# Optimization experiments

Measured on AMD Instinct MI355X. Metric: run time of the kernel, lower is better.

Reference implementation:

```python
import jax, jax.numpy as jnp
import numpy as np

D = 1024
N_HEADS = 16
HEAD = D // N_HEADS


def apply_rope(x):
    # x: [b, h, s, hd]
    b, h, s, hd = x.shape
    half = hd // 2
    pos = jnp.arange(1, s + 1, dtype=jnp.float32)  # positions start at 1 (as in source)
    thetas = 10000.0 ** (-2.0 * jnp.arange(half, dtype=jnp.float32) / hd)
    angles = pos[:, None] * thetas[None, :]  # [s, half]
    cos, sin = jnp.cos(angles), jnp.sin(angles)
    x_even, x_odd = x[..., 0::2], x[..., 1::2]
    out_even = x_even * cos - x_odd * sin
    out_odd = x_odd * cos + x_even * sin
    # interleave back: stack on new last axis then reshape
    return jnp.stack([out_even, out_odd], axis=-1).reshape(b, h, s, hd)


def setup_inputs() -> dict:
    key = jax.random.key(0)
    k1, k2, k3 = jax.random.split(key, 3)
    b, s = 4, 2048
    x = jax.random.normal(k1, (b, s, D), dtype=jnp.float32)
    # torch Linear(d, 3d, bias=False): y = x @ W.T; store as [d, 3d] so y = x @ W_qkv
    W_qkv = jax.random.normal(k2, (D, 3 * D), dtype=jnp.float32) * (1.0 / np.sqrt(D))
    W_out = jax.random.normal(k3, (D, D), dtype=jnp.float32) * (1.0 / np.sqrt(D))
    return {"x": x, "W_qkv": W_qkv, "W_out": W_out}


def reference(x, W_qkv, W_out):
    b, s, _ = x.shape
    qkv = x @ W_qkv  # [b, s, 3d]
    q, k, v = jnp.split(qkv, 3, axis=-1)

    def split_heads(t):
        return t.reshape(b, s, N_HEADS, HEAD).transpose(0, 2, 1, 3)  # [b,h,s,hd]

    q, k, v = split_heads(q), split_heads(k), split_heads(v)
    q, k = apply_rope(q), apply_rope(k)
    scale = 1.0 / np.sqrt(HEAD)
    scores = jnp.einsum("bhqd,bhkd->bhqk", q, k) * scale
    attn = jax.nn.softmax(scores, axis=-1)
    out = jnp.einsum("bhqk,bhkd->bhqd", attn, v)  # [b,h,s,hd]
    out = out.transpose(0, 2, 1, 3).reshape(b, s, D)
    return out @ W_out
```

## Files before the change

kernel.cpp:

```cpp
#include <hip/hip_runtime.h>
#include <hip/hip_bf16.h>
#include <math.h>

#define BB 4
#define SS 2048
#define DD 1024
#define NH 16
#define HD 64

typedef __attribute__((ext_vector_type(8))) short bf16x8;
typedef __attribute__((ext_vector_type(4))) float f32x4;

#define MFMA16(a, b, c) __builtin_amdgcn_mfma_f32_16x16x32_bf16(a, b, c, 0, 0, 0)

#if __has_builtin(__builtin_amdgcn_exp2f)
#define EXP2(x) __builtin_amdgcn_exp2f(x)
#else
#define EXP2(x) exp2f(x)
#endif

__device__ __forceinline__ ushort f2bf(float f) {
    unsigned int u = __builtin_bit_cast(unsigned int, f);
    u += 0x7FFF + ((u >> 16) & 1);
    return (ushort)(u >> 16);
}
__device__ __forceinline__ float bf2f(ushort u) {
    return __builtin_bit_cast(float, (unsigned)u << 16);
}
__device__ __forceinline__ unsigned pk2bf(float a, float b) {
    __hip_bfloat162 h = __float22bfloat162_rn(make_float2(a, b));
    unsigned r;
    __builtin_memcpy(&r, &h, 4);
    return r;
}

__device__ __forceinline__ void gload16(const void* g, void* l) {
    __builtin_amdgcn_global_load_lds(
        (const __attribute__((address_space(1))) void*)g,
        (__attribute__((address_space(3))) void*)l, 16, 0, 0);
}

__global__ __launch_bounds__(256)
void prep_kernel(const float* __restrict__ X, ushort* __restrict__ Xb,
                 const float* __restrict__ Wqkv, ushort* __restrict__ Wqt,
                 const float* __restrict__ Wout, ushort* __restrict__ Wot,
                 float2* __restrict__ tab)
{
    const int blk = blockIdx.x;
    const int t = threadIdx.x;
    if (blk < 4096) {
        const size_t i = ((size_t)blk * 256 + t) * 8;
        const float4 v0 = *(const float4*)&X[i];
        const float4 v1 = *(const float4*)&X[i + 4];
        uint4 o;
        o.x = pk2bf(v0.x, v0.y);
        o.y = pk2bf(v0.z, v0.w);
        o.z = pk2bf(v1.x, v1.y);
        o.w = pk2bf(v1.z, v1.w);
        *(uint4*)&Xb[i] = o;
    } else if (blk < 5120) {
        __shared__ ushort T[64][72];
        const bool isQ = blk < 4864;
        const int b2 = isQ ? blk - 4096 : blk - 4864;
        const int ncols = isQ ? 3072 : 1024;
        const float* W = isQ ? Wqkv : Wout;
        ushort* Wt = isQ ? Wqt : Wot;
        const int ki = b2 / (ncols / 64), ni = b2 % (ncols / 64);
        const int k0 = ki * 64, n0 = ni * 64;
        #pragma unroll
        for (int e = 0; e < 4; ++e) {
            const int idx = t + e * 256;
            const int kr = idx >> 4, c4 = (idx & 15) * 4;
            const float4 v = *(const float4*)&W[(size_t)(k0 + kr) * ncols + n0 + c4];
            T[c4 + 0][kr] = f2bf(v.x); T[c4 + 1][kr] = f2bf(v.y);
            T[c4 + 2][kr] = f2bf(v.z); T[c4 + 3][kr] = f2bf(v.w);
        }
        __syncthreads();
        #pragma unroll
        for (int e = 0; e < 2; ++e) {
            const int idx = t + e * 256;
            const int nr = idx >> 3, kc = (idx & 7) * 8;
            uint4 o;
            o.x = (unsigned)T[nr][kc + 0] | ((unsigned)T[nr][kc + 1] << 16);
            o.y = (unsigned)T[nr][kc + 2] | ((unsigned)T[nr][kc + 3] << 16);
            o.z = (unsigned)T[nr][kc + 4] | ((unsigned)T[nr][kc + 5] << 16);
            o.w = (unsigned)T[nr][kc + 6] | ((unsigned)T[nr][kc + 7] << 16);
            *(uint4*)&Wt[(size_t)(n0 + nr) * 1024 + k0 + kc] = o;
        }
    } else {
        const int id = (blk - 5120) * 256 + t;
        const int s = id >> 5, i = id & 31;
        const float theta = expf(-0.28782313662425572f * (float)i);
        const float ang = (float)(s + 1) * theta;
        float sn, cs;
        sincosf(ang, &sn, &cs);
        tab[id] = make_float2(cs, sn);
    }
}

__global__ __launch_bounds__(256)
void rope_cast_kernel(ushort* __restrict__ Qi, ushort* __restrict__ Ki,
                      const float2* __restrict__ tab)
{
    const int HALFT = BB * NH * SS * 8;
    const int tid = blockIdx.x * 256 + threadIdx.x;
    const bool isK = tid >= HALFT;
    const int rr = isK ? tid - HALFT : tid;
    ushort* buf = isK ? Ki : Qi;
    const float sc = isK ? 1.0f : 0.180336880111112f;

    const int row = rr >> 3;
    const int e8  = rr & 7;
    const int s   = row & (SS - 1);
    const size_t base = (size_t)row * HD + e8 * 8;
    const uint4 iv = *(const uint4*)&buf[base];
    const unsigned ua[4] = {iv.x, iv.y, iv.z, iv.w};

    uint4 o;
    unsigned ow[4];
    #pragma unroll
    for (int j = 0; j < 4; ++j) {
        const float xe = __builtin_bit_cast(float, ua[j] << 16);
        const float xo = __builtin_bit_cast(float, ua[j] & 0xffff0000u);
        const float2 cs = tab[s * 32 + e8 * 4 + j];
        const float oe = (xe * cs.x - xo * cs.y) * sc;
        const float oo = (xo * cs.x + xe * cs.y) * sc;
        ow[j] = pk2bf(oe, oo);
    }
    o.x = ow[0]; o.y = ow[1]; o.z = ow[2]; o.w = ow[3];
    *(uint4*)&buf[base] = o;
}

template<int K, int NI>
__global__ __launch_bounds__(256)
void gemm_bt_kernel(const ushort* __restrict__ Ag, const ushort* __restrict__ Btg,
                    ushort* __restrict__ D0, ushort* __restrict__ D1,
                    ushort* __restrict__ D2)
{
    __shared__ ushort Ab[2][128 * 32];
    __shared__ ushort Bb[2][128 * 32];
    const int t = threadIdx.x, lane = t & 63, w = t >> 6;
    const int lo = lane & 15, g = lane >> 4;
    const int wr = w >> 1, wc = w & 1;

    const int nwg = gridDim.x;
    const int bid = blockIdx.x;
    const int wg = (bid & 7) * (nwg >> 3) + (bid >> 3);
    const int m0 = (wg / NI) * 128, n0 = (wg % NI) * 128;

    const int srow  = lane >> 2;
    const int sslot = (lane & 3) ^ ((srow >> 1) & 3);

    f32x4 acc[4][4];
    #pragma unroll
    for (int m = 0; m < 4; ++m)
        #pragma unroll
        for (int n = 0; n < 4; ++n)
            acc[m][n] = (f32x4){0.f, 0.f, 0.f, 0.f};

#define STAGE(kt, bb)                                                              \
    {                                                                              \
        const int kk = (kt) * 32;                                                  \
        _Pragma("unroll")                                                          \
        for (int e = 0; e < 2; ++e) {                                              \
            const int r0 = w * 32 + e * 16;                                        \
            gload16(Ag  + (size_t)(m0 + r0 + srow) * K + kk + sslot * 8,           \
                    &Ab[bb][r0 * 32]);                                             \
            gload16(Btg + (size_t)(n0 + r0 + srow) * K + kk + sslot * 8,           \
                    &Bb[bb][r0 * 32]);                                             \
        }                                                                          \
    }

    const int NKS = K / 32;
    STAGE(0, 0)
    for (int kt = 0; kt < NKS; ++kt) {
        const int cur = kt & 1;
        if (kt + 1 < NKS) {
            STAGE(kt + 1, cur ^ 1)
            asm volatile("s_waitcnt vmcnt(4)" ::: "memory");
        } else {
            asm volatile("s_waitcnt vmcnt(0)" ::: "memory");
        }
        __builtin_amdgcn_sched_barrier(0);
        __builtin_amdgcn_s_barrier();

        const int xsl = ((g ^ ((lo >> 1) & 3)) << 3);
        bf16x8 af[4], bfr[4];
        #pragma unroll
        for (int m = 0; m < 4; ++m)
            af[m] = *(const bf16x8*)&Ab[cur][(wr * 64 + m * 16 + lo) * 32 + xsl];
        #pragma unroll
        for (int n = 0; n < 4; ++n)
            bfr[n] = *(const bf16x8*)&Bb[cur][(wc * 64 + n * 16 + lo) * 32 + xsl];
        #pragma unroll
        for (int m = 0; m < 4; ++m)
            #pragma unroll
            for (int n = 0; n < 4; ++n)
                acc[m][n] = MFMA16(af[m], bfr[n], acc[m][n]);

        asm volatile("s_waitcnt lgkmcnt(0)" ::: "memory");
        __builtin_amdgcn_sched_barrier(0);
        __builtin_amdgcn_s_barrier();
    }
#undef STAGE

    const int tensor = n0 >> 10;
    const int cb = n0 & 1023;
    if (tensor == 2) {
        #pragma unroll
        for (int m = 0; m < 4; ++m) {
            const int row0 = m0 + wr * 64 + m * 16 + g * 4;
            const int b = row0 >> 11, sbase = row0 & (SS - 1);
            #pragma unroll
            for (int n = 0; n < 4; ++n) {
                const int c = cb + wc * 64 + n * 16 + lo;
                const int h = c >> 6, d = c & 63;
                uint2 wv = make_uint2(pk2bf(acc[m][n][0], acc[m][n][1]),
                                      pk2bf(acc[m][n][2], acc[m][n][3]));
                *(uint2*)&D2[(((size_t)b * NH + h) * HD + d) * SS + sbase] = wv;
            }
        }
    } else {
        ushort* dst = (tensor == 0) ? D0 : D1;
        const bool evlane = (lo & 1) == 0;
        #pragma unroll
        for (int m = 0; m < 4; ++m)
            #pragma unroll
            for (int n = 0; n < 4; ++n) {
                const int c = cb + wc * 64 + n * 16 + lo;
                const int h = c >> 6, d = c & 63;
                #pragma unroll
                for (int r = 0; r < 4; ++r) {
                    const int row = m0 + wr * 64 + m * 16 + g * 4 + r;
                    const float x  = acc[m][n][r];
                    const float xp = __shfl_xor(x, 1);
                    if (evlane) {
                        const int b = row >> 11, s = row & (SS - 1);
                        *(unsigned*)&dst[(((size_t)b * NH + h) * SS + s) * HD + d] =
                            pk2bf(x, xp);
                    }
                }
            }
    }
}

template<int K>
__global__ __launch_bounds__(256)
void gemm_bt64_kernel(const ushort* __restrict__ Ag, const ushort* __restrict__ Btg,
                      float* __restrict__ Df)
{
    __shared__ ushort Ab[2][128 * 32];
    __shared__ ushort Bb[2][64 * 32];
    const int t = threadIdx.x, lane = t & 63, w = t >> 6;
    const int lo = lane & 15, g = lane >> 4;
    const int NI = 16;

    const int nwg = gridDim.x;
    const int bid = blockIdx.x;
    const int wg = (bid & 7) * (nwg >> 3) + (bid >> 3);
    const int m0 = (wg / NI) * 128, n0 = (wg % NI) * 64;

    const int srow  = lane >> 2;
    const int sslot = (lane & 3) ^ ((srow >> 1) & 3);

    f32x4 acc[2][4];
    #pragma unroll
    for (int m = 0; m < 2; ++m)
        #pragma unroll
        for (int n = 0; n < 4; ++n)
            acc[m][n] = (f32x4){0.f, 0.f, 0.f, 0.f};

#define STAGE(kt, bb)                                                              \
    {                                                                              \
        const int kk = (kt) * 32;                                                  \
        _Pragma("unroll")                                                          \
        for (int e = 0; e < 2; ++e) {                                              \
            const int r0 = w * 32 + e * 16;                                        \
            gload16(Ag + (size_t)(m0 + r0 + srow) * K + kk + sslot * 8,            \
                    &Ab[bb][r0 * 32]);                                             \
        }                                                                          \
        gload16(Btg + (size_t)(n0 + w * 16 + srow) * K + kk + sslot * 8,           \
                &Bb[bb][(w * 16) * 32]);                                           \
    }

    const int NKS = K / 32;
    STAGE(0, 0)
    for (int kt = 0; kt < NKS; ++kt) {
        const int cur = kt & 1;
        if (kt + 1 < NKS) {
            STAGE(kt + 1, cur ^ 1)
            asm volatile("s_waitcnt vmcnt(3)" ::: "memory");
        } else {
            asm volatile("s_waitcnt vmcnt(0)" ::: "memory");
        }
        __builtin_amdgcn_sched_barrier(0);
        __builtin_amdgcn_s_barrier();

        const int xsl = ((g ^ ((lo >> 1) & 3)) << 3);
        bf16x8 af[2], bfr[4];
        #pragma unroll
        for (int m = 0; m < 2; ++m)
            af[m] = *(const bf16x8*)&Ab[cur][(w * 32 + m * 16 + lo) * 32 + xsl];
        #pragma unroll
        for (int n = 0; n < 4; ++n)
            bfr[n] = *(const bf16x8*)&Bb[cur][(n * 16 + lo) * 32 + xsl];
        #pragma unroll
        for (int m = 0; m < 2; ++m)
            #pragma unroll
            for (int n = 0; n < 4; ++n)
                acc[m][n] = MFMA16(af[m], bfr[n], acc[m][n]);

        asm volatile("s_waitcnt lgkmcnt(0)" ::: "memory");
        __builtin_amdgcn_sched_barrier(0);
        __builtin_amdgcn_s_barrier();
    }
#undef STAGE

    const bool evlane = (lo & 1) == 0;
    #pragma unroll
    for (int m = 0; m < 2; ++m)
        #pragma unroll
        for (int n = 0; n < 4; ++n) {
            const int col = n0 + n * 16 + lo;
            #pragma unroll
            for (int r = 0; r < 4; ++r) {
                const int row = m0 + w * 32 + m * 16 + g * 4 + r;
                const float x  = acc[m][n][r];
                const float xp = __shfl_xor(x, 1);
                if (evlane)
                    *(float2*)&Df[(size_t)row * 1024 + col] = make_float2(x, xp);
            }
        }
}

__global__ __launch_bounds__(256, 4)
void attn_mfma_kernel(const ushort* __restrict__ Qbf, const ushort* __restrict__ Kbf,
                      const ushort* __restrict__ Vt, ushort* __restrict__ Obt)
{
    __shared__ ushort Ks[2][4096];
    __shared__ ushort Vs[2][4096];

    const int t    = threadIdx.x;
    const int lane = t & 63;
    const int w    = t >> 6;
    const int g    = lane >> 4;
    const int lo   = lane & 15;
    const int lo7  = lo & 7;

    const int i  = blockIdx.x;
    const int r_ = i & 63;
    const int bh = (r_ & 7) * 8 + (r_ >> 3);
    const int qt = i >> 6;

    const size_t kbase  = (size_t)bh * SS * HD;
    const size_t vtbase = (size_t)bh * HD * SS;
    const int s0 = qt * 128;

    bf16x8 qa[2][2];
    #pragma unroll
    for (int qh = 0; qh < 2; ++qh)
        #pragma unroll
        for (int df = 0; df < 2; ++df)
            qa[qh][df] = *(const bf16x8*)
                &Qbf[kbase + (size_t)(s0 + w * 32 + qh * 16 + lo) * HD + df * 32 + g * 8];

    f32x4 Oc[2][4];
    #pragma unroll
    for (int qh = 0; qh < 2; ++qh)
        #pragma unroll
        for (int nb = 0; nb < 4; ++nb)
            Oc[qh][nb] = (f32x4){0.f, 0.f, 0.f, 0.f};
    f32x4 lacc[2];
    lacc[0] = (f32x4){0.f, 0.f, 0.f, 0.f};
    lacc[1] = (f32x4){0.f, 0.f, 0.f, 0.f};
    const bf16x8 ones = {16256, 16256, 16256, 16256, 16256, 16256, 16256, 16256};

    const int srcsw = ((lane & 7) ^ (lane >> 3)) * 8;
    const int rowin = (lane >> 3);

    #define STAGE(kt, bb)                                                          \
    {                                                                              \
        _Pragma("unroll")                                                          \
        for (int e = 0; e < 2; ++e) {                                              \
            const int rw = w * 16 + e * 8;                                         \
            gload16(&Kbf[kbase + (size_t)((kt) * 64 + rw + rowin) * HD + srcsw],   \
                    &Ks[bb][rw * 64]);                                             \
            gload16(&Vt[vtbase + (size_t)(rw + rowin) * SS + (kt) * 64 + srcsw],   \
                    &Vs[bb][rw * 64]);                                             \
        }                                                                          \
    }

    const int NT = SS / 64;
    STAGE(0, 0)

    for (int kt = 0; kt < NT; ++kt) {
        const int cur = kt & 1;
        if (kt + 1 < NT) {
            STAGE(kt + 1, cur ^ 1)
            asm volatile("s_waitcnt vmcnt(4)" ::: "memory");
        } else {
            asm volatile("s_waitcnt vmcnt(0)" ::: "memory");
        }
        __builtin_amdgcn_sched_barrier(0);
        __builtin_amdgcn_s_barrier();

        f32x4 St[2][4];
        __builtin_amdgcn_s_setprio(1);
        #pragma unroll
        for (int k16 = 0; k16 < 4; ++k16) {
            const int row = k16 * 16 + lo;
            const int cb = row * 64;
            const bf16x8 k0 = *(const bf16x8*)&Ks[cur][cb + (((0 + g) ^ lo7) * 8)];
            const bf16x8 k1 = *(const bf16x8*)&Ks[cur][cb + (((4 + g) ^ lo7) * 8)];
            const f32x4 z = {0.f, 0.f, 0.f, 0.f};
            St[0][k16] = MFMA16(k0, qa[0][0], z);
            St[0][k16] = MFMA16(k1, qa[0][1], St[0][k16]);
            St[1][k16] = MFMA16(k0, qa[1][0], z);
            St[1][k16] = MFMA16(k1, qa[1][1], St[1][k16]);
        }
        __builtin_amdgcn_s_setprio(0);

        #pragma unroll
        for (int qh = 0; qh < 2; ++qh)
            #pragma unroll
            for (int k16 = 0; k16 < 4; ++k16)
                #pragma unroll
                for (int r = 0; r < 4; ++r)
                    St[qh][k16][r] = EXP2(St[qh][k16][r]);

        #pragma unroll
        for (int ph = 0; ph < 2; ++ph) {
            bf16x8 vf[4];
            #pragma unroll
            for (int nb = 0; nb < 4; ++nb) {
                const int rb = (nb * 16 + lo) * 64 + (g & 1) * 4;
                const uint2 vlo = *(const uint2*)
                    &Vs[cur][rb + (((ph * 4 + (g >> 1)) ^ lo7) * 8)];
                const uint2 vhi = *(const uint2*)
                    &Vs[cur][rb + (((ph * 4 + (g >> 1) + 2) ^ lo7) * 8)];
                const uint4 vv = make_uint4(vlo.x, vlo.y, vhi.x, vhi.y);
                __builtin_memcpy(&vf[nb], &vv, 16);
            }
            __builtin_amdgcn_s_setprio(1);
            #pragma unroll
            for (int qh = 0; qh < 2; ++qh) {
                uint4 pu;
                pu.x = pk2bf(St[qh][2 * ph][0], St[qh][2 * ph][1]);
                pu.y = pk2bf(St[qh][2 * ph][2], St[qh][2 * ph][3]);
                pu.z = pk2bf(St[qh][2 * ph + 1][0], St[qh][2 * ph + 1][1]);
                pu.w = pk2bf(St[qh][2 * ph + 1][2], St[qh][2 * ph + 1][3]);
                bf16x8 pa;
                __builtin_memcpy(&pa, &pu, 16);
                lacc[qh] = MFMA16(pa, ones, lacc[qh]);
                #pragma unroll
                for (int nb = 0; nb < 4; ++nb)
                    Oc[qh][nb] = MFMA16(pa, vf[nb], Oc[qh][nb]);
            }
            __builtin_amdgcn_s_setprio(0);
        }

        asm volatile("s_waitcnt lgkmcnt(0)" ::: "memory");
        __builtin_amdgcn_sched_barrier(0);
        __builtin_amdgcn_s_barrier();
    }

    const int b = bh >> 4, h = bh & 15;
    #pragma unroll
    for (int qh = 0; qh < 2; ++qh) {
        #pragma unroll
        for (int r = 0; r < 4; ++r) {
            const float inv = 1.0f / lacc[qh][r];
            const int srow = s0 + w * 32 + qh * 16 + g * 4 + r;
            const size_t rbase = (size_t)(b * SS + srow) * 1024 + h * HD;
            #pragma unroll
            for (int nb = 0; nb < 4; ++nb)
                Obt[rbase + nb * 16 + lo] = f2bf(Oc[qh][nb][r] * inv);
        }
    }
    #undef STAGE
}

extern "C" void kernel_launch(void* const* d_in, const int* in_sizes, int n_in,
                              void* d_out, int out_size, void* d_ws, size_t ws_size,
                              hipStream_t stream)
{
    const float* x    = (const float*)d_in[0];
    const float* Wqkv = (const float*)d_in[1];
    const float* Wout = (const float*)d_in[2];
    float* out = (float*)d_out;

    const size_t TEN = (size_t)BB * NH * SS * HD;
    ushort* u = (ushort*)d_ws;
    ushort* Qb16 = u;
    ushort* Kb16 = u + TEN;
    ushort* Vt   = u + 2 * TEN;
    ushort* Obt  = u + 3 * TEN;
    ushort* Xb   = u + 4 * TEN;
    ushort* Wqt  = u + 5 * TEN;
    ushort* Wot  = u + 5 * TEN + 3145728;
    float2* tab  = (float2*)(u + 5 * TEN + 3145728 + 1048576);

    prep_kernel<<<dim3(4096 + 768 + 256 + 256), 256, 0, stream>>>(
        x, Xb, Wqkv, Wqt, Wout, Wot, tab);

    gemm_bt_kernel<1024, 24><<<dim3(64 * 24), 256, 0, stream>>>(
        Xb, Wqt, Qb16, Kb16, Vt);

    rope_cast_kernel<<<dim3(2 * BB * NH * SS * 8 / 256), 256, 0, stream>>>(
        Qb16, Kb16, tab);

    attn_mfma_kernel<<<dim3(BB * NH * (SS / 128)), 256, 0, stream>>>(
        Qb16, Kb16, Vt, Obt);

    gemm_bt64_kernel<1024><<<dim3(64 * 16), 256, 0, stream>>>(Obt, Wot, out);
}
```

Before: 209.0 us.

## Fuse Q RoPE into attention kernel and pad LDS rows for K/V tiles

```diff
diff --git a/kernel.cpp b/kernel.cpp
--- a/kernel.cpp
+++ b/kernel.cpp
@@ -99,21 +99,14 @@
 }
 
 __global__ __launch_bounds__(256)
-void rope_cast_kernel(ushort* __restrict__ Qi, ushort* __restrict__ Ki,
-                      const float2* __restrict__ tab)
+void rope_k_kernel(ushort* __restrict__ Ki, const float2* __restrict__ tab)
 {
-    const int HALFT = BB * NH * SS * 8;
-    const int tid = blockIdx.x * 256 + threadIdx.x;
-    const bool isK = tid >= HALFT;
-    const int rr = isK ? tid - HALFT : tid;
-    ushort* buf = isK ? Ki : Qi;
-    const float sc = isK ? 1.0f : 0.180336880111112f;
-
+    const int rr = blockIdx.x * 256 + threadIdx.x;
     const int row = rr >> 3;
     const int e8  = rr & 7;
     const int s   = row & (SS - 1);
     const size_t base = (size_t)row * HD + e8 * 8;
-    const uint4 iv = *(const uint4*)&buf[base];
+    const uint4 iv = *(const uint4*)&Ki[base];
     const unsigned ua[4] = {iv.x, iv.y, iv.z, iv.w};
 
     uint4 o;
@@ -123,12 +116,12 @@
         const float xe = __builtin_bit_cast(float, ua[j] << 16);
         const float xo = __builtin_bit_cast(float, ua[j] & 0xffff0000u);
         const float2 cs = tab[s * 32 + e8 * 4 + j];
-        const float oe = (xe * cs.x - xo * cs.y) * sc;
-        const float oo = (xo * cs.x + xe * cs.y) * sc;
+        const float oe = xe * cs.x - xo * cs.y;
+        const float oo = xo * cs.x + xe * cs.y;
         ow[j] = pk2bf(oe, oo);
     }
     o.x = ow[0]; o.y = ow[1]; o.z = ow[2]; o.w = ow[3];
-    *(uint4*)&buf[base] = o;
+    *(uint4*)&Ki[base] = o;
 }
 
 template<int K, int NI>
@@ -335,10 +328,11 @@
 
 __global__ __launch_bounds__(256, 4)
 void attn_mfma_kernel(const ushort* __restrict__ Qbf, const ushort* __restrict__ Kbf,
-                      const ushort* __restrict__ Vt, ushort* __restrict__ Obt)
+                      const ushort* __restrict__ Vt, ushort* __restrict__ Obt,
+                      const float2* __restrict__ tab)
 {
-    __shared__ ushort Ks[2][4096];
-    __shared__ ushort Vs[2][4096];
+    __shared__ ushort Ks[2][4160];
+    __shared__ ushort Vs[2][4160];
 
     const int t    = threadIdx.x;
     const int lane = t & 63;
@@ -356,13 +350,31 @@
     const size_t vtbase = (size_t)bh * HD * SS;
     const int s0 = qt * 128;
 
+    const float QSC = 0.180336880111112f;
     bf16x8 qa[2][2];
     #pragma unroll
-    for (int qh = 0; qh < 2; ++qh)
-        #pragma unroll
-        for (int df = 0; df < 2; ++df)
-            qa[qh][df] = *(const bf16x8*)
-                &Qbf[kbase + (size_t)(s0 + w * 32 + qh * 16 + lo) * HD + df * 32 + g * 8];
+    for (int qh = 0; qh < 2; ++qh) {
+        const int srw = s0 + w * 32 + qh * 16 + lo;
+        #pragma unroll
+        for (int df = 0; df < 2; ++df) {
+            const uint4 raw = *(const uint4*)
+                &Qbf[kbase + (size_t)srw * HD + df * 32 + g * 8];
+            const unsigned ua[4] = {raw.x, raw.y, raw.z, raw.w};
+            const int ib = df * 16 + g * 4;
+            unsigned ow[4];
+            #pragma unroll
+            for (int j = 0; j < 4; ++j) {
+                const float xe = __builtin_bit_cast(float, ua[j] << 16);
+                const float xo = __builtin_bit_cast(float, ua[j] & 0xffff0000u);
+                const float2 cs = tab[srw * 32 + ib + j];
+                const float oe = (xe * cs.x - xo * cs.y) * QSC;
+                const float oo = (xo * cs.x + xe * cs.y) * QSC;
+                ow[j] = pk2bf(oe, oo);
+            }
+            const uint4 o = make_uint4(ow[0], ow[1], ow[2], ow[3]);
+            __builtin_memcpy(&qa[qh][df], &o, 16);
+        }
+    }
 
     f32x4 Oc[2][4];
     #pragma unroll
@@ -383,10 +395,11 @@
         _Pragma("unroll")                                                          \
         for (int e = 0; e < 2; ++e) {                                              \
             const int rw = w * 16 + e * 8;                                         \
+            const int dst = rw * 64 + (rw >> 3) * 8;                               \
             gload16(&Kbf[kbase + (size_t)((kt) * 64 + rw + rowin) * HD + srcsw],   \
-                    &Ks[bb][rw * 64]);                                             \
+                    &Ks[bb][dst]);                                                 \
             gload16(&Vt[vtbase + (size_t)(rw + rowin) * SS + (kt) * 64 + srcsw],   \
-                    &Vs[bb][rw * 64]);                                             \
+                    &Vs[bb][dst]);                                                 \
         }                                                                          \
     }
 
@@ -409,7 +422,7 @@
         #pragma unroll
         for (int k16 = 0; k16 < 4; ++k16) {
             const int row = k16 * 16 + lo;
-            const int cb = row * 64;
+            const int cb = row * 64 + ((row >> 3) * 8);
             const bf16x8 k0 = *(const bf16x8*)&Ks[cur][cb + (((0 + g) ^ lo7) * 8)];
             const bf16x8 k1 = *(const bf16x8*)&Ks[cur][cb + (((4 + g) ^ lo7) * 8)];
             const f32x4 z = {0.f, 0.f, 0.f, 0.f};
@@ -433,7 +446,8 @@
             bf16x8 vf[4];
             #pragma unroll
             for (int nb = 0; nb < 4; ++nb) {
-                const int rb = (nb * 16 + lo) * 64 + (g & 1) * 4;
+                const int r = nb * 16 + lo;
+                const int rb = r * 64 + ((r >> 3) * 8) + (g & 1) * 4;
                 const uint2 vlo = *(const uint2*)
                     &Vs[cur][rb + (((ph * 4 + (g >> 1)) ^ lo7) * 8)];
                 const uint2 vhi = *(const uint2*)
@@ -506,11 +520,10 @@
     gemm_bt_kernel<1024, 24><<<dim3(64 * 24), 256, 0, stream>>>(
         Xb, Wqt, Qb16, Kb16, Vt);
 
-    rope_cast_kernel<<<dim3(2 * BB * NH * SS * 8 / 256), 256, 0, stream>>>(
-        Qb16, Kb16, tab);
+    rope_k_kernel<<<dim3(BB * NH * SS * 8 / 256), 256, 0, stream>>>(Kb16, tab);
 
     attn_mfma_kernel<<<dim3(BB * NH * (SS / 128)), 256, 0, stream>>>(
-        Qb16, Kb16, Vt, Obt);
+        Qb16, Kb16, Vt, Obt, tab);
 
     gemm_bt64_kernel<1024><<<dim3(64 * 16), 256, 0, stream>>>(Obt, Wot, out);
 }
```

After: 226.4 us. +8.4%, slower.
